# Performance work log

Measured on AMD Instinct MI355X. Metric: run time of the kernel, lower is better.

## Reference

```python
import jax, jax.numpy as jnp
import numpy as np

B, T, NF, T2V, GH, NH, GRUH = 128, 256, 17, 16, 32, 4, 128


def _t2v(t, w0, b0, W, Bp):
    # t: [...] -> [..., T2V] = [linear term, sin periodic terms]
    lin = t[..., None] * w0 + b0
    per = jnp.sin(t[..., None] * W + Bp)
    return jnp.concatenate([lin, per], axis=-1)


def _gat(h, adj, W, a_src, a_dst, residual):
    # h: [N, F, Din], W: [Din, H, O], a_*: [H, O]; batched multi-head GAT over N graphs
    p = jnp.einsum('nfd,dho->nfho', h, W)
    es = jnp.einsum('nfho,ho->nhf', p, a_src)
    ed = jnp.einsum('nfho,ho->nhf', p, a_dst)
    e = jax.nn.leaky_relu(es[:, :, :, None] + ed[:, :, None, :], 0.2)  # [N,H,F,F]
    e = jnp.where(adj[None, None] > 0, e, jnp.float32(-1e9))
    a = jax.nn.softmax(e, axis=-1)
    out = jnp.einsum('nhij,njho->niho', a, p).reshape(h.shape[0], h.shape[1], -1)
    if residual:
        out = out + h
    return jax.nn.elu(out)


def _gru_dir(x, wih, whh, bih, bhh, reverse):
    # PyTorch GRU gate order [r, z, n]; x: [B,T,D] -> (outputs [B,T,H], h_final [B,H])
    gx = jnp.einsum('btd,gd->btg', x, wih) + bih
    if reverse:
        gx = gx[:, ::-1]
    H = whh.shape[1]

    def step(h, gxt):
        gh = h @ whh.T + bhh
        r = jax.nn.sigmoid(gxt[:, :H] + gh[:, :H])
        z = jax.nn.sigmoid(gxt[:, H:2 * H] + gh[:, H:2 * H])
        n = jnp.tanh(gxt[:, 2 * H:] + r * gh[:, 2 * H:])
        h2 = (1.0 - z) * n + z * h
        return h2, h2

    h0 = jnp.zeros((x.shape[0], H), x.dtype)
    hT, ys = jax.lax.scan(step, h0, jnp.swapaxes(gx, 0, 1))
    ys = jnp.swapaxes(ys, 0, 1)
    if reverse:
        ys = ys[:, ::-1]
    return ys, hT


def setup_inputs() -> dict:
    key = jax.random.key(0)
    ks = iter(jax.random.split(key, 64))

    def nrm(shape, fan):
        return jax.random.normal(next(ks), shape, jnp.float32) / np.float32(np.sqrt(fan))

    X = jax.random.normal(next(ks), (B, T, NF), jnp.float32)
    mask = (jax.random.uniform(next(ks), (B, T, NF)) > 0.3).astype(jnp.float32)
    delta = jax.random.uniform(next(ks), (B, T, NF), jnp.float32) * 10.0
    times = jnp.broadcast_to(jnp.arange(T, dtype=jnp.float32)[None], (B, T)) + jax.random.uniform(next(ks), (B, T), jnp.float32)
    adj = jnp.ones((NF, NF), jnp.float32) - jnp.eye(NF, dtype=jnp.float32)

    D0 = 2 + 2 * T2V  # node_in_dim = 34
    GO = GH * NH      # gat_out_dim = 128
    inp = dict(X=X, mask=mask, delta=delta, times=times, adj=adj,
               aw0=nrm((1,), 1), ab0=nrm((1,), 1), aW=nrm((T2V - 1,), 1), aB=nrm((T2V - 1,), 1),
               dw0=nrm((1,), 1), db0=nrm((1,), 1), dW=nrm((T2V - 1,), 1), dB=nrm((T2V - 1,), 1),
               gW0=nrm((D0, NH, GH), D0), gas0=nrm((NH, GH), GH), gad0=nrm((NH, GH), GH),
               gW1=nrm((GO, NH, GH), GO), gas1=nrm((NH, GH), GH), gad1=nrm((NH, GH), GH))
    for name, ind in [('g0f', GO), ('g0b', GO), ('g1f', 2 * GRUH), ('g1b', 2 * GRUH)]:
        inp[name + '_wih'] = nrm((3 * GRUH, ind), ind)
        inp[name + '_whh'] = nrm((3 * GRUH, GRUH), GRUH)
        inp[name + '_bih'] = jnp.zeros((3 * GRUH,), jnp.float32)
        inp[name + '_bhh'] = jnp.zeros((3 * GRUH,), jnp.float32)
    pd = 2 * GRUH
    inp.update(mh_w1=nrm((64, pd), pd), mh_b1=jnp.zeros((64,), jnp.float32),
               mh_w2=nrm((1, 64), 64), mh_b2=jnp.zeros((1,), jnp.float32),
               ch_w1=nrm((64, pd), pd), ch_b1=jnp.zeros((64,), jnp.float32),
               ch_w2=nrm((1, 64), 64), ch_b2=jnp.zeros((1,), jnp.float32))
    return inp


def reference(X, mask, delta, times, adj, aw0, ab0, aW, aB, dw0, db0, dW, dB,
              gW0, gas0, gad0, gW1, gas1, gad1,
              g0f_wih, g0f_whh, g0f_bih, g0f_bhh, g0b_wih, g0b_whh, g0b_bih, g0b_bhh,
              g1f_wih, g1f_whh, g1f_bih, g1f_bhh, g1b_wih, g1b_whh, g1b_bih, g1b_bhh,
              mh_w1, mh_b1, mh_w2, mh_b2, ch_w1, ch_b1, ch_w2, ch_b2):
    Bx, Tx, F = X.shape
    # node features: [x, mask, time2vec(t), time2vec(delta)] -> [B,T,F,34]
    t_emb = _t2v(times, aw0, ab0, aW, aB)
    t_emb = jnp.broadcast_to(t_emb[:, :, None, :], (Bx, Tx, F, T2V))
    d_emb = _t2v(delta, dw0, db0, dW, dB)
    nf = jnp.concatenate([X[..., None], mask[..., None], t_emb, d_emb], axis=-1)
    # batched GAT over all B*T graphs at once (replaces the Python bt-loop)
    h = nf.reshape(Bx * Tx, F, nf.shape[-1])
    h = _gat(h, adj, gW0, gas0, gad0, False)
    h = _gat(h, adj, gW1, gas1, gad1, True)
    z = h.mean(axis=1).reshape(Bx, Tx, NH * GH)
    # bidirectional 2-layer GRU
    yf, _ = _gru_dir(z, g0f_wih, g0f_whh, g0f_bih, g0f_bhh, False)
    yb, _ = _gru_dir(z, g0b_wih, g0b_whh, g0b_bih, g0b_bhh, True)
    y = jnp.concatenate([yf, yb], axis=-1)
    yf1, hf1 = _gru_dir(y, g1f_wih, g1f_whh, g1f_bih, g1f_bhh, False)
    yb1, hb1 = _gru_dir(y, g1b_wih, g1b_whh, g1b_bih, g1b_bhh, True)
    gru_out = jnp.concatenate([yf1, yb1], axis=-1)
    patient_emb = jnp.concatenate([hf1, hb1], axis=-1)
    m = jax.nn.relu(patient_emb @ mh_w1.T + mh_b1) @ mh_w2.T + mh_b2
    risk = jax.nn.relu(patient_emb @ ch_w1.T + ch_b1) @ ch_w2.T + ch_b2
    return (m, jax.nn.sigmoid(m), risk, patient_emb, gru_out)
```

## Files before the change

kernel.cpp:

```cpp
#include <hip/hip_runtime.h>
#include <hip/hip_bf16.h>
#include <math.h>

#define NFE 17
#define T2V 16
#define D0C 34
#define BB 128
#define TT 256
#define HH 128
#define PSTR 132
#define ASTR 136

typedef __hip_bfloat16 bf16;
__device__ __forceinline__ float b2f(bf16 x) { return __bfloat162float(x); }

typedef __attribute__((ext_vector_type(8))) __bf16 bfrag;
typedef __attribute__((ext_vector_type(4))) float  ffrag;
typedef __attribute__((ext_vector_type(4))) __bf16 bf4;

__device__ __forceinline__ float elu_fast(float v)  { return v > 0.f ? v : __expf(v) - 1.f; }
__device__ __forceinline__ float sigm_fast(float x) { return __fdividef(1.f, 1.f + __expf(-x)); }
__device__ __forceinline__ float tanh_fast(float x) {
  return __fdividef(2.f, 1.f + __expf(-2.f*x)) - 1.f;
}

__device__ __bf16 g_W0h[8192],  g_W0l[8192];
__device__ __bf16 g_W1h[16384], g_W1l[16384];

__global__ __launch_bounds__(256) void prep_w(const float* __restrict__ W0,
                                              const float* __restrict__ W1) {
  const int tid = blockIdx.x*256 + threadIdx.x;
  if (tid < 16384) {
    const int j = tid & 7, lane = (tid >> 3) & 63, ks = (tid >> 9) & 3, nt = tid >> 11;
    const int n = nt*16 + (lane & 15), k = ks*32 + (lane >> 4)*8 + j;
    const float v = W1[k*128 + n];
    const __bf16 hi = (__bf16)v;
    g_W1h[tid] = hi;
    g_W1l[tid] = (__bf16)(v - (float)hi);
  }
  if (tid < 8192) {
    const int j = tid & 7, lane = (tid >> 3) & 63, ks = (tid >> 9) & 1, nt = tid >> 10;
    const int n = nt*16 + (lane & 15), k = ks*32 + (lane >> 4)*8 + j;
    const float v = (k < D0C) ? W0[k*128 + n] : 0.f;
    const __bf16 hi = (__bf16)v;
    g_W0h[tid] = hi;
    g_W0l[tid] = (__bf16)(v - (float)hi);
  }
}

template<int KSTEPS>
__device__ __forceinline__ void gat_proj_mfma(const __bf16* s_ah, const __bf16* s_al,
                                              const __bf16* __restrict__ Wth,
                                              const __bf16* __restrict__ Wtl,
                                              float* s_p, int tid)
{
  const int lane = tid & 63, wv = tid >> 6;
  const int mn = lane & 15, q = lane >> 4;
  ffrag acc[2][2] = {};
  #pragma unroll
  for (int ks = 0; ks < KSTEPS; ++ks) {
    const bfrag ah0 = *(const bfrag*)&s_ah[(     mn)*ASTR + ks*32 + q*8];
    const bfrag al0 = *(const bfrag*)&s_al[(     mn)*ASTR + ks*32 + q*8];
    const bfrag ah1 = *(const bfrag*)&s_ah[(16 + mn)*ASTR + ks*32 + q*8];
    const bfrag al1 = *(const bfrag*)&s_al[(16 + mn)*ASTR + ks*32 + q*8];
    #pragma unroll
    for (int nt = 0; nt < 2; ++nt) {
      const int fi = (((wv*2 + nt)*KSTEPS + ks)*64 + lane)*8;
      const bfrag bh = *(const bfrag*)&Wth[fi];
      const bfrag bl = *(const bfrag*)&Wtl[fi];
      acc[0][nt] = __builtin_amdgcn_mfma_f32_16x16x32_bf16(al0, bh, acc[0][nt], 0,0,0);
      acc[0][nt] = __builtin_amdgcn_mfma_f32_16x16x32_bf16(ah0, bl, acc[0][nt], 0,0,0);
      acc[0][nt] = __builtin_amdgcn_mfma_f32_16x16x32_bf16(ah0, bh, acc[0][nt], 0,0,0);
      acc[1][nt] = __builtin_amdgcn_mfma_f32_16x16x32_bf16(al1, bh, acc[1][nt], 0,0,0);
      acc[1][nt] = __builtin_amdgcn_mfma_f32_16x16x32_bf16(ah1, bl, acc[1][nt], 0,0,0);
      acc[1][nt] = __builtin_amdgcn_mfma_f32_16x16x32_bf16(ah1, bh, acc[1][nt], 0,0,0);
    }
  }
  const int n0 = wv*32;
  #pragma unroll
  for (int nt = 0; nt < 2; ++nt) {
    const int col = n0 + nt*16 + mn;
    #pragma unroll
    for (int i = 0; i < 4; ++i)
      s_p[(q*4 + i)*PSTR + col] = acc[0][nt][i];
    if (q == 0)
      s_p[16*PSTR + col] = acc[1][nt][0];
  }
}

__device__ __forceinline__ void gat_scores(const float* s_p,
                                           const float* __restrict__ asrc,
                                           const float* __restrict__ adst,
                                           float* s_es, float* s_ed, int tid) {
  if (tid < 2*4*NFE) {
    const int which = tid >= 4*NFE;
    const int r = which ? tid - 4*NFE : tid;
    const int h = r / NFE, f = r - h*NFE;
    const float* av = which ? adst : asrc;
    float acc = 0.f;
    #pragma unroll
    for (int o = 0; o < 32; ++o)
      acc = fmaf(s_p[f*PSTR + h*32 + o], av[h*32 + o], acc);
    (which ? s_ed : s_es)[h*NFE + f] = acc;
  }
}

__device__ __forceinline__ void gat_softmax(const float* s_es, const float* s_ed,
                                            const float* s_adj,
                                            float* s_e, int tid) {
  if (tid < 4*NFE) {
    const int h = tid / NFE, i = tid - h*NFE;
    float row[NFE]; float mx = -1e30f;
    #pragma unroll
    for (int j = 0; j < NFE; ++j) {
      float v = -1.0e9f;
      if (s_adj[i*NFE + j] > 0.f) {
        float e = s_es[h*NFE + i] + s_ed[h*NFE + j];
        v = (e > 0.f) ? e : 0.2f*e;
      }
      row[j] = v; mx = fmaxf(mx, v);
    }
    float sum = 0.f;
    #pragma unroll
    for (int j = 0; j < NFE; ++j) { row[j] = __expf(row[j] - mx); sum += row[j]; }
    const float inv = __fdividef(1.f, sum);
    #pragma unroll
    for (int j = 0; j < NFE; ++j) s_e[(h*NFE + i)*NFE + j] = row[j]*inv;
  }
}

__device__ __forceinline__ void gat_out_rb(const float* s_e, const float* s_p,
                                           float* s_dst, __bf16* s_ah, __bf16* s_al,
                                           int tid) {
  const int tx = (tid & 31) * 4, ty = tid >> 5;
  const int h = tx >> 5;
  float acc[3][4];
  #pragma unroll
  for (int i = 0; i < 3; ++i)
    #pragma unroll
    for (int c = 0; c < 4; ++c) acc[i][c] = 0.f;
  for (int j = 0; j < NFE; ++j) {
    const float4 pv = *(const float4*)&s_p[j*PSTR + tx];
    #pragma unroll
    for (int i = 0; i < 3; ++i) {
      const int r = ty + 8*i;
      if (i < 2 || ty == 0) {
        const float av = s_e[(h*NFE + r)*NFE + j];
        acc[i][0] = fmaf(av, pv.x, acc[i][0]);
        acc[i][1] = fmaf(av, pv.y, acc[i][1]);
        acc[i][2] = fmaf(av, pv.z, acc[i][2]);
        acc[i][3] = fmaf(av, pv.w, acc[i][3]);
      }
    }
  }
  #pragma unroll
  for (int i = 0; i < 3; ++i) {
    const int r = ty + 8*i;
    if (i < 2 || ty == 0) {
      bf4 h4, l4;
      #pragma unroll
      for (int c = 0; c < 4; ++c) {
        const float v = elu_fast(acc[i][c]);
        s_dst[r*PSTR + tx + c] = v;
        const __bf16 hi = (__bf16)v;
        h4[c] = hi;
        l4[c] = (__bf16)(v - (float)hi);
      }
      *(bf4*)&s_ah[r*ASTR + tx] = h4;
      *(bf4*)&s_al[r*ASTR + tx] = l4;
    }
  }
}

__device__ __forceinline__ void gat_out_psum(const float* s_e, const float* s_p,
                                             const float* s_res, float* psum, int tid) {
  const int tx = (tid & 31) * 4, ty = tid >> 5;
  const int h = tx >> 5;
  float acc[3][4];
  #pragma unroll
  for (int i = 0; i < 3; ++i)
    #pragma unroll
    for (int c = 0; c < 4; ++c) acc[i][c] = 0.f;
  for (int j = 0; j < NFE; ++j) {
    const float4 pv = *(const float4*)&s_p[j*PSTR + tx];
    #pragma unroll
    for (int i = 0; i < 3; ++i) {
      const int r = ty + 8*i;
      if (i < 2 || ty == 0) {
        const float av = s_e[(h*NFE + r)*NFE + j];
        acc[i][0] = fmaf(av, pv.x, acc[i][0]);
        acc[i][1] = fmaf(av, pv.y, acc[i][1]);
        acc[i][2] = fmaf(av, pv.z, acc[i][2]);
        acc[i][3] = fmaf(av, pv.w, acc[i][3]);
      }
    }
  }
  #pragma unroll
  for (int c = 0; c < 4; ++c) psum[c] = 0.f;
  #pragma unroll
  for (int i = 0; i < 3; ++i) {
    const int r = ty + 8*i;
    if (i < 2 || ty == 0) {
      #pragma unroll
      for (int c = 0; c < 4; ++c)
        psum[c] += elu_fast(acc[i][c] + s_res[r*PSTR + tx + c]);
    }
  }
}

__global__ __launch_bounds__(256) void gat_fused(
    const float* __restrict__ X,  const float* __restrict__ Mk,
    const float* __restrict__ Dl, const float* __restrict__ Tm,
    const float* __restrict__ Adj,
    const float* __restrict__ aw0, const float* __restrict__ ab0,
    const float* __restrict__ aW,  const float* __restrict__ aB,
    const float* __restrict__ dw0, const float* __restrict__ db0,
    const float* __restrict__ dW,  const float* __restrict__ dB,
    const float* __restrict__ as0, const float* __restrict__ ad0,
    const float* __restrict__ as1, const float* __restrict__ ad1,
    float* __restrict__ zslot)
{
  __shared__ __align__(16) __bf16 s_ah[32*ASTR];
  __shared__ __align__(16) __bf16 s_al[32*ASTR];
  __shared__ __align__(16) float s_p [NFE*PSTR];
  __shared__ __align__(16) float s_h [NFE*PSTR];
  __shared__ __align__(16) float s_red[8*128];
  __shared__ float s_e [4*NFE*NFE];
  __shared__ float s_es[4*NFE];
  __shared__ float s_ed[4*NFE];
  __shared__ float s_t [T2V];
  __shared__ float s_adj[NFE*NFE];
  const int n = blockIdx.x;
  const int tid = threadIdx.x;

  {
    const float4 z4 = {0.f, 0.f, 0.f, 0.f};
    float4* za = (float4*)s_ah;
    float4* zb = (float4*)s_al;
    for (int i = tid; i < (32*ASTR*2)/16; i += 256) { za[i] = z4; zb[i] = z4; }
  }
  const float tv = Tm[n];
  if (tid < T2V) {
    s_t[tid] = (tid == 0) ? fmaf(tv, aw0[0], ab0[0])
                          : __sinf(fmaf(tv, aW[tid-1], aB[tid-1]));
  }
  for (int idx = tid; idx < NFE*NFE; idx += 256) s_adj[idx] = Adj[idx];
  __syncthreads();
  for (int idx = tid; idx < NFE*D0C; idx += 256) {
    const int f = idx / D0C, c = idx - f*D0C;
    float v;
    if (c == 0)            v = X [(size_t)n*NFE + f];
    else if (c == 1)       v = Mk[(size_t)n*NFE + f];
    else if (c < 2 + T2V)  v = s_t[c-2];
    else {
      const float dd = Dl[(size_t)n*NFE + f];
      const int j = c - (2 + T2V);
      v = (j == 0) ? fmaf(dd, dw0[0], db0[0])
                   : __sinf(fmaf(dd, dW[j-1], dB[j-1]));
    }
    const __bf16 hi = (__bf16)v;
    s_ah[f*ASTR + c] = hi;
    s_al[f*ASTR + c] = (__bf16)(v - (float)hi);
  }
  __syncthreads();
  gat_proj_mfma<2>(s_ah, s_al, g_W0h, g_W0l, s_p, tid);  __syncthreads();
  gat_scores(s_p, as0, ad0, s_es, s_ed, tid);            __syncthreads();
  gat_softmax(s_es, s_ed, s_adj, s_e, tid);              __syncthreads();
  gat_out_rb(s_e, s_p, s_h, s_ah, s_al, tid);            __syncthreads();
  gat_proj_mfma<4>(s_ah, s_al, g_W1h, g_W1l, s_p, tid);  __syncthreads();
  gat_scores(s_p, as1, ad1, s_es, s_ed, tid);            __syncthreads();
  gat_softmax(s_es, s_ed, s_adj, s_e, tid);              __syncthreads();
  {
    float psum[4];
    gat_out_psum(s_e, s_p, s_h, psum, tid);
    const int tx = (tid & 31) * 4, ty = tid >> 5;
    *(float4*)&s_red[ty*128 + tx] = *(float4*)psum;
    __syncthreads();
    if (tid < 128) {
      float acc = 0.f;
      #pragma unroll
      for (int k = 0; k < 8; ++k) acc += s_red[k*128 + tid];
      zslot[(size_t)n*256 + 128 + tid] = acc * (1.0f/17.0f);
    }
  }
}

__global__ __launch_bounds__(256) void gemm_xw_mfma(
    const float* __restrict__ A, int lda, const float* __restrict__ W,
    const float* __restrict__ bias, bf16* __restrict__ C, int K)
{
  __shared__ __bf16 Ah[64][40];
  __shared__ __bf16 Al[64][40];
  __shared__ __bf16 Wh[64][40];
  __shared__ __bf16 Wl[64][40];
  const int tid = threadIdx.x;
  const int bm0 = blockIdx.x * 64;
  const int bn0 = blockIdx.y * 64;
  const int lane = tid & 63, wv = tid >> 6;
  const int mn = lane & 15, q = lane >> 4;
  const int sr = tid >> 2, sk = (tid & 3) * 8;
  ffrag acc[4] = {};
  for (int kk = 0; kk < K; kk += 32) {
    {
      float av[8];
      *(float4*)&av[0] = *(const float4*)&A[(size_t)(bm0 + sr)*lda + kk + sk];
      *(float4*)&av[4] = *(const float4*)&A[(size_t)(bm0 + sr)*lda + kk + sk + 4];
      __bf16 th[8], tl[8];
      #pragma unroll
      for (int i = 0; i < 8; ++i) {
        const __bf16 hi = (__bf16)av[i];
        th[i] = hi;
        tl[i] = (__bf16)(av[i] - (float)hi);
      }
      *(bfrag*)&Ah[sr][sk] = *(bfrag*)th;
      *(bfrag*)&Al[sr][sk] = *(bfrag*)tl;
      float wv8[8];
      *(float4*)&wv8[0] = *(const float4*)&W[(size_t)(bn0 + sr)*K + kk + sk];
      *(float4*)&wv8[4] = *(const float4*)&W[(size_t)(bn0 + sr)*K + kk + sk + 4];
      __bf16 wh8[8], wl8[8];
      #pragma unroll
      for (int i = 0; i < 8; ++i) {
        const __bf16 hi = (__bf16)wv8[i];
        wh8[i] = hi;
        wl8[i] = (__bf16)(wv8[i] - (float)hi);
      }
      *(bfrag*)&Wh[sr][sk] = *(bfrag*)wh8;
      *(bfrag*)&Wl[sr][sk] = *(bfrag*)wl8;
    }
    __syncthreads();
    const bfrag afh = *(const bfrag*)&Ah[16*wv + mn][q*8];
    const bfrag afl = *(const bfrag*)&Al[16*wv + mn][q*8];
    #pragma unroll
    for (int t = 0; t < 4; ++t) {
      const bfrag bwh = *(const bfrag*)&Wh[16*t + mn][q*8];
      const bfrag bwl = *(const bfrag*)&Wl[16*t + mn][q*8];
      acc[t] = __builtin_amdgcn_mfma_f32_16x16x32_bf16(afl, bwh, acc[t], 0, 0, 0);
      acc[t] = __builtin_amdgcn_mfma_f32_16x16x32_bf16(afh, bwl, acc[t], 0, 0, 0);
      acc[t] = __builtin_amdgcn_mfma_f32_16x16x32_bf16(afh, bwh, acc[t], 0, 0, 0);
    }
    __syncthreads();
  }
  #pragma unroll
  for (int t = 0; t < 4; ++t) {
    const int col = bn0 + 16*t + mn;
    const float bv = bias[col];
    #pragma unroll
    for (int i = 0; i < 4; ++i) {
      const int row = bm0 + 16*wv + q*4 + i;
      C[(size_t)row*384 + col] = __float2bfloat16(acc[t][i] + bv);
    }
  }
}

__global__ __launch_bounds__(384, 1) void gru_rec(
    const bf16* __restrict__ gxf,
    const bf16* __restrict__ gxb,
    const float* __restrict__ whh_f, const float* __restrict__ whh_b,
    const float* __restrict__ bhh_f, const float* __restrict__ bhh_b,
    float* __restrict__ ys,
    float* __restrict__ hfin)
{
  const int blk = blockIdx.x;
  const int dir = blk >> 7;
  const int b   = blk & 127;
  const int g   = threadIdx.x;
  const float* whh = dir ? whh_b : whh_f;
  const float* bhh = dir ? bhh_b : bhh_f;
  const bf16* gx   = (dir ? gxb : gxf) + (size_t)b*TT*384;
  __shared__ __align__(16) float s_h[HH];
  __shared__ float s_gh[3*HH];
  __shared__ float s_gx[3*HH];
  float4 w[HH/4];
  #pragma unroll
  for (int d4 = 0; d4 < HH/4; ++d4)
    w[d4] = *(const float4*)&whh[(size_t)g*HH + 4*d4];
  const float bh = bhh[g];
  float hreg = 0.f;
  if (g < HH) s_h[g] = 0.f;
  __syncthreads();
  for (int s = 0; s < TT; ++s) {
    const int t = dir ? (TT-1-s) : s;
    const float gxv = b2f(gx[(size_t)t*384 + g]);
    float acc = bh;
    const float4* h4 = (const float4*)s_h;
    #pragma unroll
    for (int d4 = 0; d4 < HH/4; ++d4) {
      const float4 hv = h4[d4];
      acc = fmaf(hv.x, w[d4].x, acc);
      acc = fmaf(hv.y, w[d4].y, acc);
      acc = fmaf(hv.z, w[d4].z, acc);
      acc = fmaf(hv.w, w[d4].w, acc);
    }
    s_gh[g] = acc;
    s_gx[g] = gxv;
    __syncthreads();
    if (g < HH) {
      const float r  = sigm_fast(s_gx[g]    + s_gh[g]);
      const float zg = sigm_fast(s_gx[HH+g] + s_gh[HH+g]);
      const float nn = tanh_fast(s_gx[2*HH+g] + r*s_gh[2*HH+g]);
      hreg = (1.f - zg)*nn + zg*hreg;
      s_h[g] = hreg;
      ys[((size_t)b*TT + t)*256 + dir*HH + g] = hreg;
    }
    __syncthreads();
  }
  if (g < HH && hfin) hfin[(size_t)b*256 + dir*HH + g] = hreg;
}

__global__ __launch_bounds__(64) void heads_k(
    const float* __restrict__ pemb,
    const float* __restrict__ mw1, const float* __restrict__ mb1,
    const float* __restrict__ mw2, const float* __restrict__ mb2,
    const float* __restrict__ cw1, const float* __restrict__ cb1,
    const float* __restrict__ cw2, const float* __restrict__ cb2,
    float* __restrict__ out)
{
  const int b = blockIdx.x, tid = threadIdx.x;
  __shared__ float sh[64];
  const float* pe = pemb + (size_t)b*256;
  float acc = mb1[tid];
  for (int d = 0; d < 256; ++d) acc = fmaf(pe[d], mw1[(size_t)tid*256 + d], acc);
  sh[tid] = fmaxf(acc, 0.f) * mw2[tid];
  __syncthreads();
  if (tid == 0) {
    float s = mb2[0];
    for (int i = 0; i < 64; ++i) s += sh[i];
    out[b]       = s;
    out[128 + b] = 1.f/(1.f + expf(-s));
  }
  __syncthreads();
  acc = cb1[tid];
  for (int d = 0; d < 256; ++d) acc = fmaf(pe[d], cw1[(size_t)tid*256 + d], acc);
  sh[tid] = fmaxf(acc, 0.f) * cw2[tid];
  __syncthreads();
  if (tid == 0) {
    float s = cb2[0];
    for (int i = 0; i < 64; ++i) s += sh[i];
    out[256 + b] = s;
  }
}

extern "C" void kernel_launch(void* const* d_in, const int* in_sizes, int n_in,
                              void* d_out, int out_size, void* d_ws, size_t ws_size,
                              hipStream_t stream) {
  const float* X    = (const float*)d_in[0];
  const float* Mk   = (const float*)d_in[1];
  const float* Dl   = (const float*)d_in[2];
  const float* Tm   = (const float*)d_in[3];
  const float* Adj  = (const float*)d_in[4];
  const float* aw0  = (const float*)d_in[5];
  const float* ab0  = (const float*)d_in[6];
  const float* aWt  = (const float*)d_in[7];
  const float* aBt  = (const float*)d_in[8];
  const float* dw0  = (const float*)d_in[9];
  const float* db0  = (const float*)d_in[10];
  const float* dWt  = (const float*)d_in[11];
  const float* dBt  = (const float*)d_in[12];
  const float* gW0  = (const float*)d_in[13];
  const float* gas0 = (const float*)d_in[14];
  const float* gad0 = (const float*)d_in[15];
  const float* gW1  = (const float*)d_in[16];
  const float* gas1 = (const float*)d_in[17];
  const float* gad1 = (const float*)d_in[18];
  const float* g0f_wih = (const float*)d_in[19];
  const float* g0f_whh = (const float*)d_in[20];
  const float* g0f_bih = (const float*)d_in[21];
  const float* g0f_bhh = (const float*)d_in[22];
  const float* g0b_wih = (const float*)d_in[23];
  const float* g0b_whh = (const float*)d_in[24];
  const float* g0b_bih = (const float*)d_in[25];
  const float* g0b_bhh = (const float*)d_in[26];
  const float* g1f_wih = (const float*)d_in[27];
  const float* g1f_whh = (const float*)d_in[28];
  const float* g1f_bih = (const float*)d_in[29];
  const float* g1f_bhh = (const float*)d_in[30];
  const float* g1b_wih = (const float*)d_in[31];
  const float* g1b_whh = (const float*)d_in[32];
  const float* g1b_bih = (const float*)d_in[33];
  const float* g1b_bhh = (const float*)d_in[34];
  const float* mh_w1 = (const float*)d_in[35];
  const float* mh_b1 = (const float*)d_in[36];
  const float* mh_w2 = (const float*)d_in[37];
  const float* mh_b2 = (const float*)d_in[38];
  const float* ch_w1 = (const float*)d_in[39];
  const float* ch_b1 = (const float*)d_in[40];
  const float* ch_w2 = (const float*)d_in[41];
  const float* ch_b2 = (const float*)d_in[42];

  bf16* gxA = (bf16*)d_ws;
  bf16* gxB = gxA + 12582912;

  float* out  = (float*)d_out;
  float* pemb = out + 384;
  float* slot = out + 384 + 32768;

  prep_w<<<64, 256, 0, stream>>>(gW0, gW1);

  gat_fused<<<dim3(BB*TT), dim3(256), 0, stream>>>(
      X, Mk, Dl, Tm, Adj, aw0, ab0, aWt, aBt, dw0, db0, dWt, dBt,
      gas0, gad0, gas1, gad1, slot);

  dim3 ggrid(32768/64, 384/64);
  gemm_xw_mfma<<<ggrid, 256, 0, stream>>>(slot + 128, 256, g0f_wih, g0f_bih, gxA, 128);
  gemm_xw_mfma<<<ggrid, 256, 0, stream>>>(slot + 128, 256, g0b_wih, g0b_bih, gxB, 128);
  gru_rec<<<256, 384, 0, stream>>>(gxA, gxB, g0f_whh, g0b_whh, g0f_bhh, g0b_bhh,
                                   slot, nullptr);
  gemm_xw_mfma<<<ggrid, 256, 0, stream>>>(slot, 256, g1f_wih, g1f_bih, gxA, 256);
  gemm_xw_mfma<<<ggrid, 256, 0, stream>>>(slot, 256, g1b_wih, g1b_bih, gxB, 256);
  gru_rec<<<256, 384, 0, stream>>>(gxA, gxB, g1f_whh, g1b_whh, g1f_bhh, g1b_bhh,
                                   slot, pemb);

  heads_k<<<128, 64, 0, stream>>>(pemb, mh_w1, mh_b1, mh_w2, mh_b2,
                                  ch_w1, ch_b1, ch_w2, ch_b2, out);
}
```

Baseline: 1.257 ms.

## Shrink GAT shared memory, reuse split-bf16 buffers for residual, split GRU accumulators

The GAT kernel drops its separate fp32 residual buffer and rebuilds the residual from the hi/lo bf16 pair that already holds layer-one outputs. It packs all shared arrays into one aliased byte buffer, with the softmax and reduction areas sharing storage, so more blocks can fit per CU. The zero-fill loop is folded into the feature build loop, and the score dot product now uses float4 loads. The GRU recurrence splits its single FMA chain into four independent accumulators to shorten the dependency chain, which slightly changes the summation order and adds a sync before the aliased reduction buffer is reused.

```diff
diff --git a/kernel.cpp b/kernel.cpp
--- a/kernel.cpp
+++ b/kernel.cpp
@@ -99,8 +99,14 @@
     const float* av = which ? adst : asrc;
     float acc = 0.f;
     #pragma unroll
-    for (int o = 0; o < 32; ++o)
-      acc = fmaf(s_p[f*PSTR + h*32 + o], av[h*32 + o], acc);
+    for (int o = 0; o < 32; o += 4) {
+      const float4 p4 = *(const float4*)&s_p[f*PSTR + h*32 + o];
+      const float4 a4 = *(const float4*)&av[h*32 + o];
+      acc = fmaf(p4.x, a4.x, acc);
+      acc = fmaf(p4.y, a4.y, acc);
+      acc = fmaf(p4.z, a4.z, acc);
+      acc = fmaf(p4.w, a4.w, acc);
+    }
     (which ? s_ed : s_es)[h*NFE + f] = acc;
   }
 }
@@ -130,8 +136,7 @@
 }
 
 __device__ __forceinline__ void gat_out_rb(const float* s_e, const float* s_p,
-                                           float* s_dst, __bf16* s_ah, __bf16* s_al,
-                                           int tid) {
+                                           __bf16* s_ah, __bf16* s_al, int tid) {
   const int tx = (tid & 31) * 4, ty = tid >> 5;
   const int h = tx >> 5;
   float acc[3][4];
@@ -161,7 +166,6 @@
       #pragma unroll
       for (int c = 0; c < 4; ++c) {
         const float v = elu_fast(acc[i][c]);
-        s_dst[r*PSTR + tx + c] = v;
         const __bf16 hi = (__bf16)v;
         h4[c] = hi;
         l4[c] = (__bf16)(v - (float)hi);
@@ -173,7 +177,8 @@
 }
 
 __device__ __forceinline__ void gat_out_psum(const float* s_e, const float* s_p,
-                                             const float* s_res, float* psum, int tid) {
+                                             const __bf16* s_ah, const __bf16* s_al,
+                                             float* psum, int tid) {
   const int tx = (tid & 31) * 4, ty = tid >> 5;
   const int h = tx >> 5;
   float acc[3][4];
@@ -201,9 +206,13 @@
   for (int i = 0; i < 3; ++i) {
     const int r = ty + 8*i;
     if (i < 2 || ty == 0) {
+      const bf4 rh = *(const bf4*)&s_ah[r*ASTR + tx];
+      const bf4 rl = *(const bf4*)&s_al[r*ASTR + tx];
       #pragma unroll
-      for (int c = 0; c < 4; ++c)
-        psum[c] += elu_fast(acc[i][c] + s_res[r*PSTR + tx + c]);
+      for (int c = 0; c < 4; ++c) {
+        const float res = (float)rh[c] + (float)rl[c];
+        psum[c] += elu_fast(acc[i][c] + res);
+      }
     }
   }
 }
@@ -220,25 +229,19 @@
     const float* __restrict__ as1, const float* __restrict__ ad1,
     float* __restrict__ zslot)
 {
-  __shared__ __align__(16) __bf16 s_ah[32*ASTR];
-  __shared__ __align__(16) __bf16 s_al[32*ASTR];
-  __shared__ __align__(16) float s_p [NFE*PSTR];
-  __shared__ __align__(16) float s_h [NFE*PSTR];
-  __shared__ __align__(16) float s_red[8*128];
-  __shared__ float s_e [4*NFE*NFE];
-  __shared__ float s_es[4*NFE];
-  __shared__ float s_ed[4*NFE];
-  __shared__ float s_t [T2V];
-  __shared__ float s_adj[NFE*NFE];
+  __shared__ __align__(16) unsigned char smem[24624];
+  __bf16* s_ah  = (__bf16*)(smem);
+  __bf16* s_al  = (__bf16*)(smem + 4624);
+  float*  s_p   = (float*)(smem + 9248);
+  float*  s_e   = (float*)(smem + 18224);
+  float*  s_red = (float*)(smem + 18224);
+  float*  s_es  = (float*)(smem + 22848);
+  float*  s_ed  = (float*)(smem + 23120);
+  float*  s_t   = (float*)(smem + 23392);
+  float*  s_adj = (float*)(smem + 23456);
   const int n = blockIdx.x;
   const int tid = threadIdx.x;
 
-  {
-    const float4 z4 = {0.f, 0.f, 0.f, 0.f};
-    float4* za = (float4*)s_ah;
-    float4* zb = (float4*)s_al;
-    for (int i = tid; i < (32*ASTR*2)/16; i += 256) { za[i] = z4; zb[i] = z4; }
-  }
   const float tv = Tm[n];
   if (tid < T2V) {
     s_t[tid] = (tid == 0) ? fmaf(tv, aw0[0], ab0[0])
@@ -246,13 +249,13 @@
   }
   for (int idx = tid; idx < NFE*NFE; idx += 256) s_adj[idx] = Adj[idx];
   __syncthreads();
-  for (int idx = tid; idx < NFE*D0C; idx += 256) {
-    const int f = idx / D0C, c = idx - f*D0C;
-    float v;
+  for (int idx = tid; idx < NFE*64; idx += 256) {
+    const int f = idx >> 6, c = idx & 63;
+    float v = 0.f;
     if (c == 0)            v = X [(size_t)n*NFE + f];
     else if (c == 1)       v = Mk[(size_t)n*NFE + f];
     else if (c < 2 + T2V)  v = s_t[c-2];
-    else {
+    else if (c < D0C) {
       const float dd = Dl[(size_t)n*NFE + f];
       const int j = c - (2 + T2V);
       v = (j == 0) ? fmaf(dd, dw0[0], db0[0])
@@ -266,13 +269,14 @@
   gat_proj_mfma<2>(s_ah, s_al, g_W0h, g_W0l, s_p, tid);  __syncthreads();
   gat_scores(s_p, as0, ad0, s_es, s_ed, tid);            __syncthreads();
   gat_softmax(s_es, s_ed, s_adj, s_e, tid);              __syncthreads();
-  gat_out_rb(s_e, s_p, s_h, s_ah, s_al, tid);            __syncthreads();
+  gat_out_rb(s_e, s_p, s_ah, s_al, tid);                 __syncthreads();
   gat_proj_mfma<4>(s_ah, s_al, g_W1h, g_W1l, s_p, tid);  __syncthreads();
   gat_scores(s_p, as1, ad1, s_es, s_ed, tid);            __syncthreads();
   gat_softmax(s_es, s_ed, s_adj, s_e, tid);              __syncthreads();
   {
     float psum[4];
-    gat_out_psum(s_e, s_p, s_h, psum, tid);
+    gat_out_psum(s_e, s_p, s_ah, s_al, psum, tid);
+    __syncthreads();
     const int tx = (tid & 31) * 4, ty = tid >> 5;
     *(float4*)&s_red[ty*128 + tx] = *(float4*)psum;
     __syncthreads();
@@ -381,17 +385,17 @@
   for (int s = 0; s < TT; ++s) {
     const int t = dir ? (TT-1-s) : s;
     const float gxv = b2f(gx[(size_t)t*384 + g]);
-    float acc = bh;
+    float a0 = bh, a1 = 0.f, a2 = 0.f, a3 = 0.f;
     const float4* h4 = (const float4*)s_h;
     #pragma unroll
     for (int d4 = 0; d4 < HH/4; ++d4) {
       const float4 hv = h4[d4];
-      acc = fmaf(hv.x, w[d4].x, acc);
-      acc = fmaf(hv.y, w[d4].y, acc);
-      acc = fmaf(hv.z, w[d4].z, acc);
-      acc = fmaf(hv.w, w[d4].w, acc);
-    }
-    s_gh[g] = acc;
+      a0 = fmaf(hv.x, w[d4].x, a0);
+      a1 = fmaf(hv.y, w[d4].y, a1);
+      a2 = fmaf(hv.z, w[d4].z, a2);
+      a3 = fmaf(hv.w, w[d4].w, a3);
+    }
+    s_gh[g] = (a0 + a1) + (a2 + a3);
     s_gx[g] = gxv;
     __syncthreads();
     if (g < HH) {
```

After: 1.470 ms. 16.9% more time.
